# Performance work log

Measured on AMD Instinct MI355X. Metric: run time of the kernel, lower is better.

## Reference

```python
import jax, jax.numpy as jnp
import numpy as np

D = 512      # feature_bins
DK = 64      # d_k = d_v
H = 8        # n_heads
EPS = 1e-5


def setup_inputs() -> dict:
    key = jax.random.key(0)
    ks = jax.random.split(key, 12)
    B, S = 4, 2048
    s = 1.0 / np.sqrt(D)
    inp = {
        "Q": jax.random.normal(ks[0], (B, S, D), jnp.float32),
        "K": jax.random.normal(ks[1], (B, S, D), jnp.float32),
        "V": jax.random.normal(ks[2], (B, S, D), jnp.float32),
        # nn.Linear params: weight [out, in], bias [out]
        "Wq": jax.random.normal(ks[3], (H * DK, D), jnp.float32) * s,
        "bq": jnp.zeros((H * DK,), jnp.float32),
        "Wk": jax.random.normal(ks[4], (H * DK, D), jnp.float32) * s,
        "bk": jnp.zeros((H * DK,), jnp.float32),
        "Wv": jax.random.normal(ks[5], (H * DK, D), jnp.float32) * s,
        "bv": jnp.zeros((H * DK,), jnp.float32),
        "Wo": jax.random.normal(ks[6], (D, H * DK), jnp.float32) * s,
        "bo": jnp.zeros((D,), jnp.float32),
        "gamma": jnp.ones((D,), jnp.float32),
        "beta": jnp.zeros((D,), jnp.float32),
    }
    return inp


def _layernorm(x, gamma, beta):
    mu = jnp.mean(x, axis=-1, keepdims=True)
    var = jnp.mean(jnp.square(x - mu), axis=-1, keepdims=True)
    return (x - mu) * jax.lax.rsqrt(var + EPS) * gamma + beta


def reference(Q, K, V, Wq, bq, Wk, bk, Wv, bv, Wo, bo, gamma, beta):
    B, S, _ = Q.shape
    residual = Q
    # projections -> [B, H, S, DK]
    q = (Q @ Wq.T + bq).reshape(B, S, H, DK).transpose(0, 2, 1, 3)
    k = (K @ Wk.T + bk).reshape(B, S, H, DK).transpose(0, 2, 1, 3)
    v = (V @ Wv.T + bv).reshape(B, S, H, DK).transpose(0, 2, 1, 3)
    # NOTE: original code has NO 1/sqrt(d_k) scaling
    scores = jnp.einsum("bhqd,bhkd->bhqk", q, k)
    attn = jax.nn.softmax(scores, axis=-1)
    context = jnp.einsum("bhqk,bhkd->bhqd", attn, v)
    context = context.transpose(0, 2, 1, 3).reshape(B, S, H * DK)
    output = context @ Wo.T + bo
    out = _layernorm(output + residual, gamma, beta)
    return (out, attn)
```

## Files before the change

kernel.cpp:

```cpp
#include <hip/hip_runtime.h>

#define NB 4
#define NS 2048
#define ND 512
#define NH 8
#define NDK 64
#define LN_EPS 1e-5f
#define SCLAMP 80.0f

typedef __attribute__((ext_vector_type(8))) short short8;
typedef __attribute__((ext_vector_type(4))) short s16x4;
typedef __attribute__((ext_vector_type(4))) float f32x4;

__device__ inline short f2bf(float x) {
    unsigned u = __builtin_bit_cast(unsigned, x);
    unsigned r = (u + 0x7FFFu + ((u >> 16) & 1u)) >> 16;
    return (short)r;
}
__device__ inline float bf2f(short h) {
    unsigned u = ((unsigned)(unsigned short)h) << 16;
    return __builtin_bit_cast(float, u);
}
__device__ inline unsigned splitT(float x) {
    unsigned u = __builtin_bit_cast(unsigned, x);
    unsigned h = u >> 16;
    float r = x - bf2f((short)h);
    unsigned l = __builtin_bit_cast(unsigned, r) >> 16;
    return (h & 0xFFFFu) | (l << 16);
}

__device__ inline int swzS(int row, int b8) {
    return row * 64 + (((b8) * 8) ^ ((row & 7) << 3));
}
__device__ inline int swz4(int row, int g4) {
    return row * 64 + ((((g4 >> 1)) * 8) ^ ((row & 7) << 3)) + (g4 & 1) * 4;
}

template<int MODE>
__global__ __launch_bounds__(256) void k_projm(
    const float* __restrict__ X, const float* __restrict__ W,
    const float* __restrict__ bias,
    short* __restrict__ outh, short* __restrict__ outl)
{
    __shared__ short WsH[8192], WsL[8192];
    const int tid = threadIdx.x;
    const int w = tid >> 6, lane = tid & 63;
    const int lr = lane & 15, lg = lane >> 4;
    const int row0 = blockIdx.y * 64;
    const int col0 = blockIdx.x * 128;
    const int xrow = row0 + w * 16 + lr;

    f32x4 acc[8] = {};

    float4 wb[8], ab[4];
#pragma unroll
    for (int i = 0; i < 8; ++i) {
        int idx = tid + 256 * i, wrow = idx >> 4, g4 = idx & 15;
        wb[i] = *(const float4*)&W[(size_t)(col0 + wrow) * ND + g4 * 4];
    }
#pragma unroll
    for (int ks = 0; ks < 2; ++ks) {
        ab[2*ks+0] = *(const float4*)&X[(size_t)xrow * ND + ks * 32 + lg * 8];
        ab[2*ks+1] = *(const float4*)&X[(size_t)xrow * ND + ks * 32 + lg * 8 + 4];
    }

    for (int kc = 0; kc < 8; ++kc) {
        __syncthreads();
#pragma unroll
        for (int i = 0; i < 8; ++i) {
            int idx = tid + 256 * i, wrow = idx >> 4, g4 = idx & 15;
            s16x4 hv, lv;
            unsigned p0 = splitT(wb[i].x), p1 = splitT(wb[i].y);
            unsigned p2 = splitT(wb[i].z), p3 = splitT(wb[i].w);
            hv[0] = (short)p0; lv[0] = (short)(p0 >> 16);
            hv[1] = (short)p1; lv[1] = (short)(p1 >> 16);
            hv[2] = (short)p2; lv[2] = (short)(p2 >> 16);
            hv[3] = (short)p3; lv[3] = (short)(p3 >> 16);
            int off = swz4(wrow, g4);
            *(s16x4*)&WsH[off] = hv;
            *(s16x4*)&WsL[off] = lv;
        }
        __syncthreads();

        short8 ah[2], al[2];
#pragma unroll
        for (int ks = 0; ks < 2; ++ks) {
#pragma unroll
            for (int j = 0; j < 4; ++j) {
                unsigned p = splitT(ab[2*ks][j]);
                ah[ks][j] = (short)p; al[ks][j] = (short)(p >> 16);
            }
#pragma unroll
            for (int j = 0; j < 4; ++j) {
                unsigned p = splitT(ab[2*ks+1][j]);
                ah[ks][4+j] = (short)p; al[ks][4+j] = (short)(p >> 16);
            }
        }

        if (kc < 7) {
            const int kn = (kc + 1) * 64;
#pragma unroll
            for (int i = 0; i < 8; ++i) {
                int idx = tid + 256 * i, wrow = idx >> 4, g4 = idx & 15;
                wb[i] = *(const float4*)&W[(size_t)(col0 + wrow) * ND + kn + g4 * 4];
            }
#pragma unroll
            for (int ks = 0; ks < 2; ++ks) {
                ab[2*ks+0] = *(const float4*)&X[(size_t)xrow * ND + kn + ks * 32 + lg * 8];
                ab[2*ks+1] = *(const float4*)&X[(size_t)xrow * ND + kn + ks * 32 + lg * 8 + 4];
            }
        }

#pragma unroll
        for (int cs = 0; cs < 8; ++cs)
#pragma unroll
            for (int ks = 0; ks < 2; ++ks) {
                short8 fh = *(const short8*)&WsH[swzS(cs * 16 + lr, ks * 4 + lg)];
                short8 fl = *(const short8*)&WsL[swzS(cs * 16 + lr, ks * 4 + lg)];
                acc[cs] = __builtin_amdgcn_mfma_f32_16x16x32_bf16(ah[ks], fh, acc[cs], 0, 0, 0);
                acc[cs] = __builtin_amdgcn_mfma_f32_16x16x32_bf16(ah[ks], fl, acc[cs], 0, 0, 0);
                acc[cs] = __builtin_amdgcn_mfma_f32_16x16x32_bf16(al[ks], fh, acc[cs], 0, 0, 0);
            }
    }

#pragma unroll
    for (int cs = 0; cs < 8; ++cs) {
        int c = col0 + cs * 16 + lr;
        int h_ = c >> 6, dk = c & (NDK - 1);
        float bv = bias[c];
#pragma unroll
        for (int r = 0; r < 4; ++r) {
            int gr = row0 + w * 16 + lg * 4 + r;
            int b_ = gr >> 11, s_ = gr & (NS - 1);
            float x = acc[cs][r] + bv;
            if (MODE == 0) {
                size_t idx = (((size_t)b_ * NH + h_) * NS + s_) * NDK + dk;
                short hb = f2bf(x);
                outh[idx] = hb;
                outl[idx] = f2bf(x - bf2f(hb));
            } else {
                size_t idx = (((size_t)b_ * NH + h_) * NDK + dk) * NS + s_;
                outh[idx] = f2bf(x);
            }
        }
    }
}

__device__ inline void att_decode2(int wg, int& bh, int& rt) {
    rt = (wg >> 3) & 15;
    bh = (wg & 7) + ((wg >> 7) << 3);
}

__global__ __launch_bounds__(256) void k_pvl(
    const short* __restrict__ qh, const short* __restrict__ ql,
    const short* __restrict__ kh, const short* __restrict__ kl,
    const short* __restrict__ vtb,
    float* __restrict__ iLrow, short* __restrict__ ctxb)
{
    __shared__ short KsH[4096], KsL[4096], Vs[4096];
    __shared__ short plbf[4][32][72];
    const int tid = threadIdx.x;
    const int w = tid >> 6, lane = tid & 63;
    const int lr = lane & 15, lg = lane >> 4;
    int bh, rt;
    att_decode2(blockIdx.x, bh, rt);
    const int row0 = rt * 128 + w * 16;
    const size_t base = (size_t)bh * NS * NDK;
    const short* vb = vtb + (size_t)bh * NDK * NS;
    const int srow0 = tid >> 3, sb8 = tid & 7;
    const int srow1 = srow0 + 32;

    short8 ah[2][2], al[2][2];
#pragma unroll
    for (int st = 0; st < 2; ++st)
#pragma unroll
        for (int ks = 0; ks < 2; ++ks) {
            size_t idx = base + (size_t)(row0 + st * 64 + lr) * NDK + ks * 32 + lg * 8;
            ah[st][ks] = *(const short8*)&qh[idx];
            al[st][ks] = *(const short8*)&ql[idx];
        }

    float lsum[2][4] = {};
    f32x4 vacc[2][4] = {};

    short8 nh0, nh1, nl0, nl1, nv0, nv1;
    {
        nh0 = *(const short8*)&kh[base + (size_t)(srow0) * NDK + sb8 * 8];
        nh1 = *(const short8*)&kh[base + (size_t)(srow1) * NDK + sb8 * 8];
        nl0 = *(const short8*)&kl[base + (size_t)(srow0) * NDK + sb8 * 8];
        nl1 = *(const short8*)&kl[base + (size_t)(srow1) * NDK + sb8 * 8];
        nv0 = *(const short8*)&vb[(size_t)srow0 * NS + sb8 * 8];
        nv1 = *(const short8*)&vb[(size_t)srow1 * NS + sb8 * 8];
    }

    for (int c = 0; c < 32; ++c) {
        short8 ch0 = nh0, ch1 = nh1, cl0 = nl0, cl1 = nl1, cv0 = nv0, cv1 = nv1;
        __syncthreads();
        *(short8*)&KsH[swzS(srow0, sb8)] = ch0;
        *(short8*)&KsH[swzS(srow1, sb8)] = ch1;
        *(short8*)&KsL[swzS(srow0, sb8)] = cl0;
        *(short8*)&KsL[swzS(srow1, sb8)] = cl1;
        *(short8*)&Vs[swzS(srow0, sb8)] = cv0;
        *(short8*)&Vs[swzS(srow1, sb8)] = cv1;
        __syncthreads();

        if (c < 31) {
            const int coln = (c + 1) * 64;
            nh0 = *(const short8*)&kh[base + (size_t)(coln + srow0) * NDK + sb8 * 8];
            nh1 = *(const short8*)&kh[base + (size_t)(coln + srow1) * NDK + sb8 * 8];
            nl0 = *(const short8*)&kl[base + (size_t)(coln + srow0) * NDK + sb8 * 8];
            nl1 = *(const short8*)&kl[base + (size_t)(coln + srow1) * NDK + sb8 * 8];
            nv0 = *(const short8*)&vb[(size_t)srow0 * NS + coln + sb8 * 8];
            nv1 = *(const short8*)&vb[(size_t)srow1 * NS + coln + sb8 * 8];
        }

        f32x4 sa[2][4] = {};
#pragma unroll
        for (int cs = 0; cs < 4; ++cs)
#pragma unroll
            for (int ks = 0; ks < 2; ++ks) {
                short8 fh = *(const short8*)&KsH[swzS(cs * 16 + lr, ks * 4 + lg)];
                short8 fl = *(const short8*)&KsL[swzS(cs * 16 + lr, ks * 4 + lg)];
#pragma unroll
                for (int st = 0; st < 2; ++st) {
                    sa[st][cs] = __builtin_amdgcn_mfma_f32_16x16x32_bf16(ah[st][ks], fh, sa[st][cs], 0, 0, 0);
                    sa[st][cs] = __builtin_amdgcn_mfma_f32_16x16x32_bf16(ah[st][ks], fl, sa[st][cs], 0, 0, 0);
                    sa[st][cs] = __builtin_amdgcn_mfma_f32_16x16x32_bf16(al[st][ks], fh, sa[st][cs], 0, 0, 0);
                }
            }

#pragma unroll
        for (int st = 0; st < 2; ++st)
#pragma unroll
            for (int cs = 0; cs < 4; ++cs)
#pragma unroll
                for (int r = 0; r < 4; ++r) {
                    float e = __expf(fminf(sa[st][cs][r], SCLAMP));
                    lsum[st][r] += e;
                    plbf[w][st * 16 + lg * 4 + r][cs * 16 + lr] = f2bf(e);
                }

#pragma unroll
        for (int k2 = 0; k2 < 2; ++k2) {
            short8 pa0 = *(const short8*)&plbf[w][lr][k2 * 32 + lg * 8];
            short8 pa1 = *(const short8*)&plbf[w][16 + lr][k2 * 32 + lg * 8];
#pragma unroll
            for (int d = 0; d < 4; ++d) {
                short8 vf = *(const short8*)&Vs[swzS(d * 16 + lr, k2 * 4 + lg)];
                vacc[0][d] = __builtin_amdgcn_mfma_f32_16x16x32_bf16(pa0, vf, vacc[0][d], 0, 0, 0);
                vacc[1][d] = __builtin_amdgcn_mfma_f32_16x16x32_bf16(pa1, vf, vacc[1][d], 0, 0, 0);
            }
        }
    }

#pragma unroll
    for (int st = 0; st < 2; ++st)
#pragma unroll
        for (int r = 0; r < 4; ++r)
#pragma unroll
            for (int off = 1; off < 16; off <<= 1)
                lsum[st][r] += __shfl_xor(lsum[st][r], off);

    float iL[2][4];
#pragma unroll
    for (int st = 0; st < 2; ++st)
#pragma unroll
        for (int r = 0; r < 4; ++r) iL[st][r] = 1.0f / lsum[st][r];
    if (lr == 0) {
#pragma unroll
        for (int st = 0; st < 2; ++st)
#pragma unroll
            for (int r = 0; r < 4; ++r)
                iLrow[(size_t)bh * NS + row0 + st * 64 + lg * 4 + r] = iL[st][r];
    }
    const int b_ = bh >> 3, h_ = bh & 7;
#pragma unroll
    for (int st = 0; st < 2; ++st)
#pragma unroll
        for (int d = 0; d < 4; ++d)
#pragma unroll
            for (int r = 0; r < 4; ++r) {
                int row = row0 + st * 64 + lg * 4 + r;
                ctxb[((size_t)b_ * NS + row) * ND + h_ * NDK + d * 16 + lr] =
                    f2bf(vacc[st][d][r] * iL[st][r]);
            }
}

__global__ __launch_bounds__(256) void k_attn_write(
    const short* __restrict__ qh, const short* __restrict__ ql,
    const short* __restrict__ kh, const short* __restrict__ kl,
    const float* __restrict__ iLrow, float* __restrict__ attn)
{
    __shared__ short KsH[4096], KsL[4096];
    const int tid = threadIdx.x;
    const int w = tid >> 6, lane = tid & 63;
    const int lr = lane & 15, lg = lane >> 4;
    int bh, rt;
    att_decode2(blockIdx.x, bh, rt);
    const int row0 = rt * 128 + w * 16;
    const size_t base = (size_t)bh * NS * NDK;
    float* ab = attn + (size_t)bh * NS * NS;
    const int srow0 = tid >> 3, sb8 = tid & 7;
    const int srow1 = srow0 + 32;

    short8 ah[2][2], al[2][2];
#pragma unroll
    for (int st = 0; st < 2; ++st)
#pragma unroll
        for (int ks = 0; ks < 2; ++ks) {
            size_t idx = base + (size_t)(row0 + st * 64 + lr) * NDK + ks * 32 + lg * 8;
            ah[st][ks] = *(const short8*)&qh[idx];
            al[st][ks] = *(const short8*)&ql[idx];
        }
    float iLr[2][4];
#pragma unroll
    for (int st = 0; st < 2; ++st)
#pragma unroll
        for (int r = 0; r < 4; ++r)
            iLr[st][r] = iLrow[(size_t)bh * NS + row0 + st * 64 + lg * 4 + r];

    short8 nh0, nh1, nl0, nl1;
    {
        nh0 = *(const short8*)&kh[base + (size_t)(srow0) * NDK + sb8 * 8];
        nh1 = *(const short8*)&kh[base + (size_t)(srow1) * NDK + sb8 * 8];
        nl0 = *(const short8*)&kl[base + (size_t)(srow0) * NDK + sb8 * 8];
        nl1 = *(const short8*)&kl[base + (size_t)(srow1) * NDK + sb8 * 8];
    }

    for (int c = 0; c < 32; ++c) {
        short8 ch0 = nh0, ch1 = nh1, cl0 = nl0, cl1 = nl1;
        __syncthreads();
        *(short8*)&KsH[swzS(srow0, sb8)] = ch0;
        *(short8*)&KsH[swzS(srow1, sb8)] = ch1;
        *(short8*)&KsL[swzS(srow0, sb8)] = cl0;
        *(short8*)&KsL[swzS(srow1, sb8)] = cl1;
        __syncthreads();

        if (c < 31) {
            const int coln = (c + 1) * 64;
            nh0 = *(const short8*)&kh[base + (size_t)(coln + srow0) * NDK + sb8 * 8];
            nh1 = *(const short8*)&kh[base + (size_t)(coln + srow1) * NDK + sb8 * 8];
            nl0 = *(const short8*)&kl[base + (size_t)(coln + srow0) * NDK + sb8 * 8];
            nl1 = *(const short8*)&kl[base + (size_t)(coln + srow1) * NDK + sb8 * 8];
        }

        const int col0 = c * 64;
        f32x4 sa[2][4] = {};
#pragma unroll
        for (int cs = 0; cs < 4; ++cs)
#pragma unroll
            for (int ks = 0; ks < 2; ++ks) {
                short8 fh = *(const short8*)&KsH[swzS(cs * 16 + lr, ks * 4 + lg)];
                short8 fl = *(const short8*)&KsL[swzS(cs * 16 + lr, ks * 4 + lg)];
#pragma unroll
                for (int st = 0; st < 2; ++st) {
                    sa[st][cs] = __builtin_amdgcn_mfma_f32_16x16x32_bf16(ah[st][ks], fh, sa[st][cs], 0, 0, 0);
                    sa[st][cs] = __builtin_amdgcn_mfma_f32_16x16x32_bf16(ah[st][ks], fl, sa[st][cs], 0, 0, 0);
                    sa[st][cs] = __builtin_amdgcn_mfma_f32_16x16x32_bf16(al[st][ks], fh, sa[st][cs], 0, 0, 0);
                }
            }

#pragma unroll
        for (int st = 0; st < 2; ++st)
#pragma unroll
            for (int cs = 0; cs < 4; ++cs)
#pragma unroll
                for (int r = 0; r < 4; ++r) {
                    float p = __expf(fminf(sa[st][cs][r], SCLAMP)) * iLr[st][r];
                    ab[(size_t)(row0 + st * 64 + lg * 4 + r) * NS + col0 + cs * 16 + lr] = p;
                }
    }
}

__global__ __launch_bounds__(256) void k_outproj_m(
    const short* __restrict__ Xc, const float* __restrict__ W,
    const float* __restrict__ bias, const float* __restrict__ Qin,
    float* __restrict__ out)
{
    __shared__ short WsH[8192], WsL[8192];
    const int tid = threadIdx.x;
    const int w = tid >> 6, lane = tid & 63;
    const int lr = lane & 15, lg = lane >> 4;
    const int row0 = blockIdx.y * 64;
    const int col0 = blockIdx.x * 128;
    const int xrow = row0 + w * 16 + lr;

    f32x4 acc[8] = {};

    float4 wb[8];
    short8 abn[2];
#pragma unroll
    for (int i = 0; i < 8; ++i) {
        int idx = tid + 256 * i, wrow = idx >> 4, g4 = idx & 15;
        wb[i] = *(const float4*)&W[(size_t)(col0 + wrow) * ND + g4 * 4];
    }
#pragma unroll
    for (int ks = 0; ks < 2; ++ks)
        abn[ks] = *(const short8*)&Xc[(size_t)xrow * ND + ks * 32 + lg * 8];

    for (int kc = 0; kc < 8; ++kc) {
        __syncthreads();
#pragma unroll
        for (int i = 0; i < 8; ++i) {
            int idx = tid + 256 * i, wrow = idx >> 4, g4 = idx & 15;
            s16x4 hv, lv;
            unsigned p0 = splitT(wb[i].x), p1 = splitT(wb[i].y);
            unsigned p2 = splitT(wb[i].z), p3 = splitT(wb[i].w);
            hv[0] = (short)p0; lv[0] = (short)(p0 >> 16);
            hv[1] = (short)p1; lv[1] = (short)(p1 >> 16);
            hv[2] = (short)p2; lv[2] = (short)(p2 >> 16);
            hv[3] = (short)p3; lv[3] = (short)(p3 >> 16);
            int off = swz4(wrow, g4);
            *(s16x4*)&WsH[off] = hv;
            *(s16x4*)&WsL[off] = lv;
        }
        __syncthreads();

        short8 ah[2] = { abn[0], abn[1] };

        if (kc < 7) {
            const int kn = (kc + 1) * 64;
#pragma unroll
            for (int i = 0; i < 8; ++i) {
                int idx = tid + 256 * i, wrow = idx >> 4, g4 = idx & 15;
                wb[i] = *(const float4*)&W[(size_t)(col0 + wrow) * ND + kn + g4 * 4];
            }
#pragma unroll
            for (int ks = 0; ks < 2; ++ks)
                abn[ks] = *(const short8*)&Xc[(size_t)xrow * ND + kn + ks * 32 + lg * 8];
        }

#pragma unroll
        for (int cs = 0; cs < 8; ++cs)
#pragma unroll
            for (int ks = 0; ks < 2; ++ks) {
                short8 fh = *(const short8*)&WsH[swzS(cs * 16 + lr, ks * 4 + lg)];
                short8 fl = *(const short8*)&WsL[swzS(cs * 16 + lr, ks * 4 + lg)];
                acc[cs] = __builtin_amdgcn_mfma_f32_16x16x32_bf16(ah[ks], fh, acc[cs], 0, 0, 0);
                acc[cs] = __builtin_amdgcn_mfma_f32_16x16x32_bf16(ah[ks], fl, acc[cs], 0, 0, 0);
            }
    }

#pragma unroll
    for (int cs = 0; cs < 8; ++cs) {
        int c = col0 + cs * 16 + lr;
        float bv = bias[c];
#pragma unroll
        for (int r = 0; r < 4; ++r) {
            int gr = row0 + w * 16 + lg * 4 + r;
            float res = Qin[(size_t)gr * ND + c];
            out[(size_t)gr * ND + c] = acc[cs][r] + bv + res;
        }
    }
}

__global__ __launch_bounds__(256) void k_ln(
    float* __restrict__ out, const float* __restrict__ gamma,
    const float* __restrict__ beta)
{
    const int tid = threadIdx.x;
    float* p = out + (size_t)blockIdx.x * ND;
    float2 v = *(const float2*)&p[tid * 2];

    float s = v.x + v.y;
#pragma unroll
    for (int off = 32; off > 0; off >>= 1) s += __shfl_xor(s, off);
    __shared__ float red1[4];
    __shared__ float red2[4];
    if ((tid & 63) == 0) red1[tid >> 6] = s;
    __syncthreads();
    const float mu = (red1[0] + red1[1] + red1[2] + red1[3]) * (1.0f / ND);

    float dx = v.x - mu, dy = v.y - mu;
    float q = dx * dx + dy * dy;
#pragma unroll
    for (int off = 32; off > 0; off >>= 1) q += __shfl_xor(q, off);
    if ((tid & 63) == 0) red2[tid >> 6] = q;
    __syncthreads();
    const float var = (red2[0] + red2[1] + red2[2] + red2[3]) * (1.0f / ND);
    const float inv = rsqrtf(var + LN_EPS);

    float2 g = *(const float2*)&gamma[tid * 2];
    float2 be = *(const float2*)&beta[tid * 2];
    float2 o = { dx * inv * g.x + be.x, dy * inv * g.y + be.y };
    *(float2*)&p[tid * 2] = o;
}

extern "C" void kernel_launch(void* const* d_in, const int* in_sizes, int n_in,
                              void* d_out, int out_size, void* d_ws, size_t ws_size,
                              hipStream_t stream)
{
    const float* Q    = (const float*)d_in[0];
    const float* K    = (const float*)d_in[1];
    const float* V    = (const float*)d_in[2];
    const float* Wq   = (const float*)d_in[3];
    const float* bq   = (const float*)d_in[4];
    const float* Wk   = (const float*)d_in[5];
    const float* bk   = (const float*)d_in[6];
    const float* Wv   = (const float*)d_in[7];
    const float* bv   = (const float*)d_in[8];
    const float* Wo   = (const float*)d_in[9];
    const float* bo   = (const float*)d_in[10];
    const float* gam  = (const float*)d_in[11];
    const float* bet  = (const float*)d_in[12];

    float* out  = (float*)d_out;
    float* attn = out + (size_t)NB * NS * ND;

    const size_t QKV = (size_t)NB * NH * NS * NDK;
    short* qh   = (short*)d_ws;
    short* ql   = qh + QKV;
    short* kh   = ql + QKV;
    short* kl   = kh + QKV;
    short* vtb  = kl + QKV;
    short* ctxb = vtb + QKV;
    float* iLrow = (float*)(ctxb + QKV);

    dim3 blk(256);

    dim3 gP(ND / 128, (NB * NS) / 64);
    k_projm<0><<<gP, blk, 0, stream>>>(Q, Wq, bq, qh, ql);
    k_projm<0><<<gP, blk, 0, stream>>>(K, Wk, bk, kh, kl);
    k_projm<1><<<gP, blk, 0, stream>>>(V, Wv, bv, vtb, (short*)nullptr);

    dim3 gAtt((NS / 128) * NB * NH);
    k_pvl<<<gAtt, blk, 0, stream>>>(qh, ql, kh, kl, vtb, iLrow, ctxb);
    k_attn_write<<<gAtt, blk, 0, stream>>>(qh, ql, kh, kl, iLrow, attn);

    dim3 gO(ND / 128, (NB * NS) / 64);
    k_outproj_m<<<gO, blk, 0, stream>>>(ctxb, Wo, bo, Q, out);

    k_ln<<<dim3(NB * NS), blk, 0, stream>>>(out, gam, bet);
}
```

Before: 332.0 us.

## Merge QKV projections into one launch, add MFMA priority hints, nontemporal attn stores

Folds the three separate Q/K/V projection launches into a single kernel that uses blockIdx.z to pick the input, weights and output layout. This removes two launch gaps and lets the three projections share the GPU. It also wraps the MFMA loops in s_setprio(1)/(0) so waves issuing matrix work get scheduling priority, and writes the large attention-probability matrix with nontemporal stores to avoid polluting cache. The z-dependent pointer selection adds a little uniform branching per block.

```diff
diff --git a/kernel.cpp b/kernel.cpp
--- a/kernel.cpp
+++ b/kernel.cpp
@@ -36,13 +36,24 @@
     return row * 64 + ((((g4 >> 1)) * 8) ^ ((row & 7) << 3)) + (g4 & 1) * 4;
 }
 
-template<int MODE>
-__global__ __launch_bounds__(256) void k_projm(
-    const float* __restrict__ X, const float* __restrict__ W,
-    const float* __restrict__ bias,
-    short* __restrict__ outh, short* __restrict__ outl)
+__global__ __launch_bounds__(256) void k_projm_all(
+    const float* __restrict__ Qx, const float* __restrict__ Kx,
+    const float* __restrict__ Vx,
+    const float* __restrict__ Wq, const float* __restrict__ bq,
+    const float* __restrict__ Wk, const float* __restrict__ bk,
+    const float* __restrict__ Wv, const float* __restrict__ bv,
+    short* __restrict__ qh, short* __restrict__ ql,
+    short* __restrict__ kh, short* __restrict__ kl,
+    short* __restrict__ vtb)
 {
     __shared__ short WsH[8192], WsL[8192];
+    const int which = blockIdx.z;
+    const float* X    = which == 0 ? Qx : (which == 1 ? Kx : Vx);
+    const float* W    = which == 0 ? Wq : (which == 1 ? Wk : Wv);
+    const float* bias = which == 0 ? bq : (which == 1 ? bk : bv);
+    short* outh       = which == 0 ? qh : (which == 1 ? kh : vtb);
+    short* outl       = which == 0 ? ql : kl;
+
     const int tid = threadIdx.x;
     const int w = tid >> 6, lane = tid & 63;
     const int lr = lane & 15, lg = lane >> 4;
@@ -111,6 +122,7 @@
             }
         }
 
+        __builtin_amdgcn_s_setprio(1);
 #pragma unroll
         for (int cs = 0; cs < 8; ++cs)
 #pragma unroll
@@ -121,6 +133,7 @@
                 acc[cs] = __builtin_amdgcn_mfma_f32_16x16x32_bf16(ah[ks], fl, acc[cs], 0, 0, 0);
                 acc[cs] = __builtin_amdgcn_mfma_f32_16x16x32_bf16(al[ks], fh, acc[cs], 0, 0, 0);
             }
+        __builtin_amdgcn_s_setprio(0);
     }
 
 #pragma unroll
@@ -133,7 +146,7 @@
             int gr = row0 + w * 16 + lg * 4 + r;
             int b_ = gr >> 11, s_ = gr & (NS - 1);
             float x = acc[cs][r] + bv;
-            if (MODE == 0) {
+            if (which != 2) {
                 size_t idx = (((size_t)b_ * NH + h_) * NS + s_) * NDK + dk;
                 short hb = f2bf(x);
                 outh[idx] = hb;
@@ -215,6 +228,7 @@
         }
 
         f32x4 sa[2][4] = {};
+        __builtin_amdgcn_s_setprio(1);
 #pragma unroll
         for (int cs = 0; cs < 4; ++cs)
 #pragma unroll
@@ -228,6 +242,7 @@
                     sa[st][cs] = __builtin_amdgcn_mfma_f32_16x16x32_bf16(al[st][ks], fh, sa[st][cs], 0, 0, 0);
                 }
             }
+        __builtin_amdgcn_s_setprio(0);
 
 #pragma unroll
         for (int st = 0; st < 2; ++st)
@@ -240,6 +255,7 @@
                     plbf[w][st * 16 + lg * 4 + r][cs * 16 + lr] = f2bf(e);
                 }
 
+        __builtin_amdgcn_s_setprio(1);
 #pragma unroll
         for (int k2 = 0; k2 < 2; ++k2) {
             short8 pa0 = *(const short8*)&plbf[w][lr][k2 * 32 + lg * 8];
@@ -251,6 +267,7 @@
                 vacc[1][d] = __builtin_amdgcn_mfma_f32_16x16x32_bf16(pa1, vf, vacc[1][d], 0, 0, 0);
             }
         }
+        __builtin_amdgcn_s_setprio(0);
     }
 
 #pragma unroll
@@ -346,6 +363,7 @@
 
         const int col0 = c * 64;
         f32x4 sa[2][4] = {};
+        __builtin_amdgcn_s_setprio(1);
 #pragma unroll
         for (int cs = 0; cs < 4; ++cs)
 #pragma unroll
@@ -359,6 +377,7 @@
                     sa[st][cs] = __builtin_amdgcn_mfma_f32_16x16x32_bf16(al[st][ks], fh, sa[st][cs], 0, 0, 0);
                 }
             }
+        __builtin_amdgcn_s_setprio(0);
 
 #pragma unroll
         for (int st = 0; st < 2; ++st)
@@ -367,7 +386,8 @@
 #pragma unroll
                 for (int r = 0; r < 4; ++r) {
                     float p = __expf(fminf(sa[st][cs][r], SCLAMP)) * iLr[st][r];
-                    ab[(size_t)(row0 + st * 64 + lg * 4 + r) * NS + col0 + cs * 16 + lr] = p;
+                    __builtin_nontemporal_store(
+                        p, &ab[(size_t)(row0 + st * 64 + lg * 4 + r) * NS + col0 + cs * 16 + lr]);
                 }
     }
 }
@@ -430,6 +450,7 @@
                 abn[ks] = *(const short8*)&Xc[(size_t)xrow * ND + kn + ks * 32 + lg * 8];
         }
 
+        __builtin_amdgcn_s_setprio(1);
 #pragma unroll
         for (int cs = 0; cs < 8; ++cs)
 #pragma unroll
@@ -439,6 +460,7 @@
                 acc[cs] = __builtin_amdgcn_mfma_f32_16x16x32_bf16(ah[ks], fh, acc[cs], 0, 0, 0);
                 acc[cs] = __builtin_amdgcn_mfma_f32_16x16x32_bf16(ah[ks], fl, acc[cs], 0, 0, 0);
             }
+        __builtin_amdgcn_s_setprio(0);
     }
 
 #pragma unroll
@@ -518,10 +540,9 @@
 
     dim3 blk(256);
 
-    dim3 gP(ND / 128, (NB * NS) / 64);
-    k_projm<0><<<gP, blk, 0, stream>>>(Q, Wq, bq, qh, ql);
-    k_projm<0><<<gP, blk, 0, stream>>>(K, Wk, bk, kh, kl);
-    k_projm<1><<<gP, blk, 0, stream>>>(V, Wv, bv, vtb, (short*)nullptr);
+    dim3 gP(ND / 128, (NB * NS) / 64, 3);
+    k_projm_all<<<gP, blk, 0, stream>>>(Q, K, V, Wq, bq, Wk, bk, Wv, bv,
+                                        qh, ql, kh, kl, vtb);
 
     dim3 gAtt((NS / 128) * NB * NH);
     k_pvl<<<gAtt, blk, 0, stream>>>(qh, ql, kh, kl, vtb, iLrow, ctxb);
```

Measured after the change: 365.7 us. 10.1% more time.
